# Kernel optimization log

Hardware: AMD Instinct MI355X
Metric: run time of the kernel (lower is better)

Reference implementation:

```python
import jax, jax.numpy as jnp
import numpy as np

N, E, F, H, G, C = 50000, 800000, 128, 64, 512, 10
RATIO = 0.5  # forward arg `ratio` baked as constant


def seg_mean(msgs, idx, n):
    s = jax.ops.segment_sum(msgs, idx, num_segments=n)
    cnt = jax.ops.segment_sum(jnp.ones(idx.shape[0], msgs.dtype), idx, num_segments=n)
    return s / jnp.maximum(cnt, 1.0)[:, None]


def sage(x, src, dst, Wl, bl, Wr, ew=None):
    # PyG SAGEConv: lin_l(mean_{j->i} msg_j) + lin_r(x_i); weighted variant scales messages
    m = x[src] if ew is None else x[src] * ew[:, None]
    agg = seg_mean(m, dst, x.shape[0])
    return agg @ Wl + bl + x @ Wr


def topk_mask(scores, seg, num_graphs, ratio):
    # per-graph (segment) top-k edge selection: keep ceil(ratio*edges_in_graph) highest scores
    e = scores.shape[0]
    counts = jax.ops.segment_sum(jnp.ones(e, jnp.float32), seg, num_segments=num_graphs)
    order = jnp.lexsort((-scores, seg))  # sort by segment, then score descending
    seg_sorted = seg[order]
    starts = jnp.concatenate([jnp.zeros(1, jnp.float32), jnp.cumsum(counts)[:-1]])
    rank = jnp.arange(e, dtype=jnp.float32) - starts[seg_sorted]
    k = jnp.ceil(ratio * counts)
    sel = (rank < k[seg_sorted]).astype(scores.dtype)
    return jnp.zeros(e, scores.dtype).at[order].set(sel)


def setup_inputs():
    key = jax.random.key(0)
    ks = jax.random.split(key, 16)
    w = lambda k, shape, fan: (jax.random.normal(k, shape, jnp.float32) / np.sqrt(fan))
    return {
        'x': jax.random.normal(ks[0], (N, F), jnp.float32),
        'edge_index': jax.random.randint(ks[1], (2, E), 0, N, jnp.int32),
        'batch': jnp.sort(jax.random.randint(ks[2], (N,), 0, G, jnp.int32)),
        'W1l': w(ks[3], (F, H), F), 'b1l': jnp.zeros(H, jnp.float32), 'W1r': w(ks[4], (F, H), F),
        'W2l': w(ks[5], (H, H), H), 'b2l': jnp.zeros(H, jnp.float32), 'W2r': w(ks[6], (H, H), H),
        'W3l': w(ks[7], (H, H), H), 'b3l': jnp.zeros(H, jnp.float32), 'W3r': w(ks[8], (H, H), H),
        'Wlin1': w(ks[9], (H, H), H), 'blin1': jnp.zeros(H, jnp.float32),
        'Wlin2': w(ks[10], (H, C), H), 'blin2': jnp.zeros(C, jnp.float32),
    }


def reference(x, edge_index, batch, W1l, b1l, W1r, W2l, b2l, W2r, W3l, b3l, W3r, Wlin1, blin1, Wlin2, blin2):
    src, dst = edge_index[0], edge_index[1]
    h = jax.nn.relu(sage(x, src, dst, W1l, b1l, W1r))
    edge_scores = jnp.sum(h[src] * h[dst], axis=-1)  # [E]
    seg = batch[src]  # graph id per edge (sections)
    sampled = topk_mask(edge_scores, seg, G, RATIO)
    ew = edge_scores * sampled
    h = jax.nn.relu(sage(h, src, dst, W2l, b2l, W2r, ew))
    h = jax.nn.relu(sage(h, src, dst, W3l, b3l, W3r, ew))
    pooled = seg_mean(h, batch, G)  # global_mean_pool
    z = jax.nn.relu(pooled @ Wlin1 + blin1)
    z = z @ Wlin2 + blin2  # dropout inactive in eval
    return jax.nn.log_softmax(z, axis=-1), sampled
```

## Files before the change

kernel.cpp:

```cpp
#include <hip/hip_runtime.h>
#include <hip/hip_bf16.h>
#include <math.h>

static constexpr int N = 50000;
static constexpr int E = 800000;
static constexpr int F = 128;
static constexpr int H = 64;
static constexpr int G = 512;
static constexpr int C = 10;
static constexpr int CAP = 256;

static inline int cdiv(long a, int b) { return (int)((a + b - 1) / b); }

__device__ __forceinline__ float uinv_score(unsigned u) {
  return (u & 0x80000000u) ? __uint_as_float(u & 0x7fffffffu) : __uint_as_float(~u);
}

__global__ void k_deg_goff(const int* __restrict__ dst, const int* __restrict__ batch,
                           int* __restrict__ deg, int* __restrict__ goff) {
  for (int i = blockIdx.x * 256 + threadIdx.x; i < N; i += gridDim.x * 256) {
    int b = batch[i];
    if (i == 0) {
      for (int g = 0; g <= b; ++g) goff[g] = 0;
    } else {
      int p = batch[i - 1];
      for (int g = p + 1; g <= b; ++g) goff[g] = i;
    }
    if (i == N - 1) {
      for (int g = b + 1; g <= G; ++g) goff[g] = N;
    }
  }
  for (int e = blockIdx.x * 256 + threadIdx.x; e < E; e += gridDim.x * 256)
    atomicAdd(&deg[dst[e]], 1);
}

__global__ void k_scan_a(const int* __restrict__ cnt, int* __restrict__ off,
                         int* __restrict__ bsum, int n) {
  __shared__ int wsum[16];
  int tid = threadIdx.x, lane = tid & 63, wv = tid >> 6;
  int idx = blockIdx.x * 4096 + tid * 4;
  int v0 = (idx + 0 < n) ? cnt[idx + 0] : 0;
  int v1 = (idx + 1 < n) ? cnt[idx + 1] : 0;
  int v2 = (idx + 2 < n) ? cnt[idx + 2] : 0;
  int v3 = (idx + 3 < n) ? cnt[idx + 3] : 0;
  int local = v0 + v1 + v2 + v3;
  int inc = local;
  for (int d = 1; d < 64; d <<= 1) {
    int t = __shfl_up(inc, d);
    if (lane >= d) inc += t;
  }
  if (lane == 63) wsum[wv] = inc;
  __syncthreads();
  if (tid < 16) {
    int t = wsum[tid];
    for (int d = 1; d < 16; d <<= 1) {
      int u = __shfl_up(t, d);
      if (tid >= d) t += u;
    }
    wsum[tid] = t;
  }
  __syncthreads();
  int woff = (wv > 0) ? wsum[wv - 1] : 0;
  int excl = woff + inc - local;
  if (idx + 0 < n) off[idx + 0] = excl;
  if (idx + 1 < n) off[idx + 1] = excl + v0;
  if (idx + 2 < n) off[idx + 2] = excl + v0 + v1;
  if (idx + 3 < n) off[idx + 3] = excl + v0 + v1 + v2;
  if (tid == 0) bsum[blockIdx.x] = wsum[15];
}

__global__ void k_scan_b(int* __restrict__ bsum, int nb) {
  int lane = threadIdx.x;
  int v = (lane < nb) ? bsum[lane] : 0;
  int inc = v;
  for (int d = 1; d < 64; d <<= 1) {
    int t = __shfl_up(inc, d);
    if (lane >= d) inc += t;
  }
  if (lane < nb) bsum[lane] = inc - v;
  if (lane == nb) bsum[nb] = inc;
}

__global__ void k_scan_c(int* __restrict__ off, int* __restrict__ cursor,
                         const int* __restrict__ bsum, int n, int nb) {
  int i = blockIdx.x * 256 + threadIdx.x;
  if (i < n) {
    int v = off[i] + bsum[i >> 12];
    off[i] = v;
    cursor[i] = v;
  } else if (i == n) {
    off[n] = bsum[nb];
  }
}

__global__ void k_fill_csr(const int* __restrict__ src, const int* __restrict__ dst,
                           int* __restrict__ cursor, int2* __restrict__ csr,
                           int* __restrict__ einv, int lo, int hi) {
  int e = blockIdx.x * 256 + threadIdx.x;
  if (e >= E) return;
  int d = dst[e];
  if (d < lo || d >= hi) return;
  int slot = atomicAdd(&cursor[d], 1);
  csr[slot] = make_int2(src[e], e);
  einv[e] = slot;
}

template <int K>
__global__ void k_gemm2(const float* __restrict__ in, const float* __restrict__ Wl,
                        const float* __restrict__ Wr, const float* __restrict__ b,
                        float* __restrict__ y, float* __restrict__ r) {
  __shared__ float sx[16][K];
  int lane = threadIdx.x, ty = threadIdx.y;
  int tid = ty * 64 + lane;
  int row0 = blockIdx.x * 16;
  const float4* gsrc = (const float4*)(in + (size_t)row0 * K);
  float4* sdst = (float4*)(&sx[0][0]);
#pragma unroll
  for (int i = tid; i < 16 * K / 4; i += 256) sdst[i] = gsrc[i];
  __syncthreads();
  float al[4], ar[4];
  float bias = b[lane];
#pragma unroll
  for (int j = 0; j < 4; ++j) { al[j] = 0.f; ar[j] = bias; }
#pragma unroll 4
  for (int f = 0; f < K; ++f) {
    float wl = Wl[f * H + lane];
    float wr = Wr[f * H + lane];
#pragma unroll
    for (int j = 0; j < 4; ++j) {
      float xv = sx[ty * 4 + j][f];
      al[j] += xv * wl;
      ar[j] += xv * wr;
    }
  }
#pragma unroll
  for (int j = 0; j < 4; ++j) {
    int row = row0 + ty * 4 + j;
    y[(size_t)row * H + lane] = al[j];
    r[(size_t)row * H + lane] = ar[j];
  }
}

template <int K>
__global__ void k_gemm2h(const float* __restrict__ in, const float* __restrict__ Wl,
                         const float* __restrict__ Wr, const float* __restrict__ b,
                         __hip_bfloat16* __restrict__ y, float* __restrict__ r) {
  __shared__ float sx[16][K];
  int lane = threadIdx.x, ty = threadIdx.y;
  int tid = ty * 64 + lane;
  int row0 = blockIdx.x * 16;
  const float4* gsrc = (const float4*)(in + (size_t)row0 * K);
  float4* sdst = (float4*)(&sx[0][0]);
#pragma unroll
  for (int i = tid; i < 16 * K / 4; i += 256) sdst[i] = gsrc[i];
  __syncthreads();
  float al[4], ar[4];
  float bias = b[lane];
#pragma unroll
  for (int j = 0; j < 4; ++j) { al[j] = 0.f; ar[j] = bias; }
#pragma unroll 4
  for (int f = 0; f < K; ++f) {
    float wl = Wl[f * H + lane];
    float wr = Wr[f * H + lane];
#pragma unroll
    for (int j = 0; j < 4; ++j) {
      float xv = sx[ty * 4 + j][f];
      al[j] += xv * wl;
      ar[j] += xv * wr;
    }
  }
#pragma unroll
  for (int j = 0; j < 4; ++j) {
    int row = row0 + ty * 4 + j;
    y[(size_t)row * H + lane] = __float2bfloat16(al[j]);
    r[(size_t)row * H + lane] = ar[j];
  }
}

__global__ void k_agg1(const float* __restrict__ y, const float* __restrict__ r,
                       const int2* __restrict__ csr, const int* __restrict__ off,
                       float* __restrict__ out) {
  int node = blockIdx.x * 8 + threadIdx.y;
  int lane = threadIdx.x;
  int q = lane >> 3, c = lane & 7;
  int s0 = off[node], s1 = off[node + 1];
  float4 a0 = make_float4(0.f, 0.f, 0.f, 0.f);
  float4 a1 = make_float4(0.f, 0.f, 0.f, 0.f);
  int i = s0 + q;
  for (; i + 8 < s1; i += 16) {
    int2 se0 = csr[i];
    int2 se1 = csr[i + 8];
    const float4* p0 = (const float4*)(y + (size_t)se0.x * H);
    const float4* p1 = (const float4*)(y + (size_t)se1.x * H);
    float4 u0 = p0[c], v0 = p0[c + 8];
    float4 u1 = p1[c], v1 = p1[c + 8];
    a0.x += u0.x + u1.x; a0.y += u0.y + u1.y; a0.z += u0.z + u1.z; a0.w += u0.w + u1.w;
    a1.x += v0.x + v1.x; a1.y += v0.y + v1.y; a1.z += v0.z + v1.z; a1.w += v0.w + v1.w;
  }
  for (; i < s1; i += 8) {
    int2 se = csr[i];
    const float4* p = (const float4*)(y + (size_t)se.x * H);
    float4 u = p[c], v = p[c + 8];
    a0.x += u.x; a0.y += u.y; a0.z += u.z; a0.w += u.w;
    a1.x += v.x; a1.y += v.y; a1.z += v.z; a1.w += v.w;
  }
#pragma unroll
  for (int d = 8; d < 64; d <<= 1) {
    a0.x += __shfl_xor(a0.x, d); a0.y += __shfl_xor(a0.y, d);
    a0.z += __shfl_xor(a0.z, d); a0.w += __shfl_xor(a0.w, d);
    a1.x += __shfl_xor(a1.x, d); a1.y += __shfl_xor(a1.y, d);
    a1.z += __shfl_xor(a1.z, d); a1.w += __shfl_xor(a1.w, d);
  }
  if (q == 0) {
    float inv = 1.f / fmaxf((float)(s1 - s0), 1.f);
    const float4* rp = (const float4*)(r + (size_t)node * H);
    float4 r0 = rp[c], r1 = rp[c + 8];
    float4 o0, o1;
    o0.x = fmaxf(a0.x * inv + r0.x, 0.f); o0.y = fmaxf(a0.y * inv + r0.y, 0.f);
    o0.z = fmaxf(a0.z * inv + r0.z, 0.f); o0.w = fmaxf(a0.w * inv + r0.w, 0.f);
    o1.x = fmaxf(a1.x * inv + r1.x, 0.f); o1.y = fmaxf(a1.y * inv + r1.y, 0.f);
    o1.z = fmaxf(a1.z * inv + r1.z, 0.f); o1.w = fmaxf(a1.w * inv + r1.w, 0.f);
    float4* op = (float4*)(out + (size_t)node * H);
    op[c] = o0; op[c + 8] = o1;
  }
}

__global__ void k_compact(const unsigned char* __restrict__ sel,
                          const int2* __restrict__ csr, const float* __restrict__ ewc,
                          const int* __restrict__ off, int2* __restrict__ csr2,
                          int* __restrict__ cnt2) {
  int node = blockIdx.x * 8 + threadIdx.y;
  int lane = threadIdx.x;
  int s0 = off[node], s1 = off[node + 1];
  unsigned long long lt = ((unsigned long long)1 << lane) - 1;
  int cum = 0;
  for (int i0 = s0; i0 < s1; i0 += 64) {
    int i = i0 + lane;
    bool f = (i < s1) && sel[i];
    unsigned long long m = __ballot(f);
    if (f) {
      int rank = __popcll(m & lt);
      int2 se = csr[i];
      csr2[s0 + cum + rank] = make_int2(se.x, __float_as_int(ewc[i]));
    }
    cum += __popcll(m);
  }
  if (lane == 0) cnt2[node] = cum;
}

__global__ void k_agg_w(const __hip_bfloat16* __restrict__ y, const float* __restrict__ r,
                        const int2* __restrict__ csr2, const int* __restrict__ cnt2,
                        const int* __restrict__ off, float* __restrict__ out) {
  int node = blockIdx.x * 8 + threadIdx.y;
  int lane = threadIdx.x;
  int q = lane >> 3, c = lane & 7;
  int b0 = off[node], cn = cnt2[node];
  float a[8] = {0.f, 0.f, 0.f, 0.f, 0.f, 0.f, 0.f, 0.f};
  for (int j = q; j < cn; j += 8) {
    int2 sw = csr2[b0 + j];
    float w = __int_as_float(sw.y);
    uint4 pk = ((const uint4*)((const unsigned short*)y + (size_t)sw.x * H))[c];
    a[0] += w * __uint_as_float(pk.x << 16); a[1] += w * __uint_as_float(pk.x & 0xffff0000u);
    a[2] += w * __uint_as_float(pk.y << 16); a[3] += w * __uint_as_float(pk.y & 0xffff0000u);
    a[4] += w * __uint_as_float(pk.z << 16); a[5] += w * __uint_as_float(pk.z & 0xffff0000u);
    a[6] += w * __uint_as_float(pk.w << 16); a[7] += w * __uint_as_float(pk.w & 0xffff0000u);
  }
#pragma unroll
  for (int d = 8; d < 64; d <<= 1) {
#pragma unroll
    for (int j = 0; j < 8; ++j) a[j] += __shfl_xor(a[j], d);
  }
  if (q == 0) {
    int degn = off[node + 1] - off[node];
    float inv = 1.f / fmaxf((float)degn, 1.f);
    const float4* rp = (const float4*)(r + (size_t)node * H);
    float4 r0 = rp[2 * c], r1 = rp[2 * c + 1];
    float4 o0, o1;
    o0.x = fmaxf(a[0] * inv + r0.x, 0.f); o0.y = fmaxf(a[1] * inv + r0.y, 0.f);
    o0.z = fmaxf(a[2] * inv + r0.z, 0.f); o0.w = fmaxf(a[3] * inv + r0.w, 0.f);
    o1.x = fmaxf(a[4] * inv + r1.x, 0.f); o1.y = fmaxf(a[5] * inv + r1.y, 0.f);
    o1.z = fmaxf(a[6] * inv + r1.z, 0.f); o1.w = fmaxf(a[7] * inv + r1.w, 0.f);
    float4* op = (float4*)(out + (size_t)node * H);
    op[2 * c] = o0; op[2 * c + 1] = o1;
  }
}

__global__ void k_score_csr(const float* __restrict__ h1, const int2* __restrict__ csr,
                            const int* __restrict__ off, const int* __restrict__ batch,
                            unsigned* __restrict__ scoreu_csr,
                            unsigned short* __restrict__ seg_csr, int* __restrict__ hist) {
  int node = blockIdx.x * 8 + threadIdx.y;
  int lane = threadIdx.x;
  int q = lane >> 4, c = lane & 15;
  int s0 = off[node], s1 = off[node + 1];
  float4 hn = ((const float4*)(h1 + (size_t)node * H))[c];
  int i = s0 + q;
  for (; i + 4 < s1; i += 8) {
    int2 se0 = csr[i];
    int2 se1 = csr[i + 4];
    float4 hs0 = ((const float4*)(h1 + (size_t)se0.x * H))[c];
    float4 hs1 = ((const float4*)(h1 + (size_t)se1.x * H))[c];
    float p0 = hn.x * hs0.x + hn.y * hs0.y + hn.z * hs0.z + hn.w * hs0.w;
    float p1 = hn.x * hs1.x + hn.y * hs1.y + hn.z * hs1.z + hn.w * hs1.w;
    p0 += __shfl_xor(p0, 1); p1 += __shfl_xor(p1, 1);
    p0 += __shfl_xor(p0, 2); p1 += __shfl_xor(p1, 2);
    p0 += __shfl_xor(p0, 4); p1 += __shfl_xor(p1, 4);
    p0 += __shfl_xor(p0, 8); p1 += __shfl_xor(p1, 8);
    if (c == 0) {
      int g0 = batch[se0.x], g1 = batch[se1.x];
      unsigned u0 = __float_as_uint(p0); u0 = (u0 & 0x80000000u) ? ~u0 : (u0 | 0x80000000u);
      unsigned u1 = __float_as_uint(p1); u1 = (u1 & 0x80000000u) ? ~u1 : (u1 | 0x80000000u);
      scoreu_csr[i] = u0; scoreu_csr[i + 4] = u1;
      seg_csr[i] = (unsigned short)g0; seg_csr[i + 4] = (unsigned short)g1;
      atomicAdd(&hist[g0 * 256 + (int)(u0 >> 24)], 1);
      atomicAdd(&hist[g1 * 256 + (int)(u1 >> 24)], 1);
    }
  }
  for (; i < s1; i += 4) {
    int2 se = csr[i];
    float4 hs = ((const float4*)(h1 + (size_t)se.x * H))[c];
    float p = hn.x * hs.x + hn.y * hs.y + hn.z * hs.z + hn.w * hs.w;
    p += __shfl_xor(p, 1);
    p += __shfl_xor(p, 2);
    p += __shfl_xor(p, 4);
    p += __shfl_xor(p, 8);
    if (c == 0) {
      int g = batch[se.x];
      unsigned u = __float_as_uint(p);
      u = (u & 0x80000000u) ? ~u : (u | 0x80000000u);
      scoreu_csr[i] = u;
      seg_csr[i] = (unsigned short)g;
      atomicAdd(&hist[g * 256 + (int)(u >> 24)], 1);
    }
  }
}

__global__ void k_hist(const unsigned* __restrict__ scoreu, const unsigned short* __restrict__ seg,
                       const unsigned* __restrict__ prefix, int* __restrict__ hist, int pass) {
  int e = blockIdx.x * 256 + threadIdx.x;
  if (e >= E) return;
  unsigned u = scoreu[e];
  int g = (int)seg[e];
  int predshift = 32 - 8 * pass;
  if ((u >> predshift) == (prefix[g] >> predshift))
    atomicAdd(&hist[g * 256 + (int)((u >> (24 - 8 * pass)) & 0xFFu)], 1);
}

__global__ void k_scan(int* __restrict__ hist, unsigned* __restrict__ prefix,
                       int* __restrict__ krem, int pass) {
  int g = blockIdx.x;
  int lane = threadIdx.x;
  int4* row = (int4*)(hist + (size_t)g * 256);
  int4 v = row[lane];
  int vj[4] = {v.x, v.y, v.z, v.w};
  int s = v.x + v.y + v.z + v.w;
  int inc = s;
  for (int d = 1; d < 64; d <<= 1) {
    int t = __shfl_up(inc, d);
    if (lane >= d) inc += t;
  }
  int T = __shfl(inc, 63);
  int k = (pass == 0) ? ((T + 1) >> 1) : krem[g];
  int excl = inc - s;
  int pre[4] = {excl, excl + vj[0], excl + vj[0] + vj[1], excl + vj[0] + vj[1] + vj[2]};
  int bsel_l = -1, newk_l = 0;
  if (k > 0) {
    for (int j = 3; j >= 0; --j) {
      int suf = T - pre[j];
      if (suf >= k) { bsel_l = 4 * lane + j; newk_l = k - (suf - vj[j]); break; }
    }
  }
  unsigned long long mask = __ballot(bsel_l >= 0);
  int bsel = 255, newk = 0;
  if (k > 0 && mask) {
    int hi = 63 - __builtin_clzll(mask);
    bsel = __shfl(bsel_l, hi);
    newk = __shfl(newk_l, hi);
  }
  if (lane == 0) {
    unsigned base = (pass == 0) ? 0u : prefix[g];
    prefix[g] = base | ((unsigned)bsel << (24 - 8 * pass));
    krem[g] = newk;
  }
  row[lane] = make_int4(0, 0, 0, 0);
}

__global__ void k_select(const unsigned* __restrict__ scoreu_csr,
                         const unsigned short* __restrict__ seg_csr,
                         const unsigned* __restrict__ thresh,
                         int* __restrict__ eqcnt, int* __restrict__ eqlist,
                         unsigned char* __restrict__ sel_csr, float* __restrict__ ew_csr) {
  int s = blockIdx.x * 256 + threadIdx.x;
  if (s >= E) return;
  unsigned u = scoreu_csr[s];
  int g = (int)seg_csr[s];
  unsigned t = thresh[g];
  unsigned um = u & 0xffffff00u;
  float sel = 0.f;
  if (um > t) sel = 1.f;
  else if (um == t) {
    int slot = atomicAdd(&eqcnt[g], 1);
    if (slot < CAP) eqlist[g * CAP + slot] = s;
  }
  sel_csr[s] = (unsigned char)sel;
  ew_csr[s] = uinv_score(u) * sel;
}

__global__ void k_resolve(const int* __restrict__ krem, const int* __restrict__ eqcnt,
                          const int* __restrict__ eqlist, const int2* __restrict__ csr,
                          const unsigned* __restrict__ scoreu_csr,
                          unsigned char* __restrict__ sel_csr, float* __restrict__ ew_csr) {
  int g = blockIdx.x * 256 + threadIdx.x;
  if (g >= G) return;
  int c = eqcnt[g]; if (c > CAP) c = CAP;
  int r = krem[g];  if (r > c) r = c;
  const int* lst = eqlist + g * CAP;
  unsigned last_u = 0u; int last_e = -1; bool first = true;
  for (int i = 0; i < r; ++i) {
    unsigned bu = 0u; int be = -1, bs = -1;
    for (int j = 0; j < c; ++j) {
      int slot = lst[j];
      unsigned u = scoreu_csr[slot];
      int eid = csr[slot].y;
      bool after = first || (u < last_u) || (u == last_u && eid > last_e);
      if (after && (bs < 0 || u > bu || (u == bu && eid < be))) { bu = u; be = eid; bs = slot; }
    }
    if (bs < 0) break;
    sel_csr[bs] = 1;
    ew_csr[bs] = uinv_score(bu);
    last_u = bu; last_e = be; first = false;
  }
}

__global__ void k_sampled(const int* __restrict__ einv, const unsigned char* __restrict__ sel_csr,
                          float* __restrict__ sampled) {
  int e = (blockIdx.x * 256 + threadIdx.x) * 4;
  if (e >= E) return;
  int4 iv = *(const int4*)(einv + e);
  float4 o;
  o.x = (float)sel_csr[iv.x];
  o.y = (float)sel_csr[iv.y];
  o.z = (float)sel_csr[iv.z];
  o.w = (float)sel_csr[iv.w];
  *(float4*)(sampled + e) = o;
}

__global__ void k_poolhead(const float* __restrict__ h3, const int* __restrict__ goff,
                           const float* __restrict__ W1, const float* __restrict__ b1,
                           const float* __restrict__ W2, const float* __restrict__ b2,
                           float* __restrict__ outp) {
  int g = blockIdx.x;
  int h = threadIdx.x;
  int s0 = goff[g], s1 = goff[g + 1];
  float a = 0.f;
  for (int n = s0; n < s1; ++n) a += h3[(size_t)n * H + h];
  float inv = 1.f / fmaxf((float)(s1 - s0), 1.f);
  __shared__ float p[H], z1[H], z2[C];
  __shared__ float lse;
  p[h] = a * inv;
  __syncthreads();
  float acc = b1[h];
#pragma unroll 8
  for (int f = 0; f < H; ++f) acc += p[f] * W1[f * H + h];
  z1[h] = fmaxf(acc, 0.f);
  __syncthreads();
  if (h < C) {
    float a2 = b2[h];
#pragma unroll 8
    for (int f = 0; f < H; ++f) a2 += z1[f] * W2[f * C + h];
    z2[h] = a2;
  }
  __syncthreads();
  if (h == 0) {
    float m = z2[0];
    for (int c = 1; c < C; ++c) m = fmaxf(m, z2[c]);
    float s = 0.f;
    for (int c = 0; c < C; ++c) s += expf(z2[c] - m);
    lse = m + logf(s);
  }
  __syncthreads();
  if (h < C) outp[(size_t)g * C + h] = z2[h] - lse;
}

extern "C" void kernel_launch(void* const* d_in, const int* in_sizes, int n_in,
                              void* d_out, int out_size, void* d_ws, size_t ws_size,
                              hipStream_t stream) {
  const float* x     = (const float*)d_in[0];
  const int*   ei    = (const int*)d_in[1];
  const int*   batch = (const int*)d_in[2];
  const float* W1l   = (const float*)d_in[3];
  const float* b1l   = (const float*)d_in[4];
  const float* W1r   = (const float*)d_in[5];
  const float* W2l   = (const float*)d_in[6];
  const float* b2l   = (const float*)d_in[7];
  const float* W2r   = (const float*)d_in[8];
  const float* W3l   = (const float*)d_in[9];
  const float* b3l   = (const float*)d_in[10];
  const float* W3r   = (const float*)d_in[11];
  const float* Wlin1 = (const float*)d_in[12];
  const float* blin1 = (const float*)d_in[13];
  const float* Wlin2 = (const float*)d_in[14];
  const float* blin2 = (const float*)d_in[15];

  const int* srcv = ei;
  const int* dstv = ei + E;

  float* out_ls   = (float*)d_out;
  float* out_samp = out_ls + G * C;

  char* w = (char*)d_ws;
  auto carve = [&](size_t bytes) { void* p = (void*)w; w += (bytes + 255) & ~(size_t)255; return p; };
  char* zbase   = w;
  int*      deg     = (int*)carve((size_t)N * 4);
  int*      eqcnt   = (int*)carve((size_t)G * 4);
  int*      hist    = (int*)carve((size_t)G * 256 * 4);
  size_t    zbytes  = (size_t)(w - zbase);
  float*    h1      = (float*)carve((size_t)N * H * 4);
  float*    h2      = (float*)carve((size_t)N * H * 4);
  float*    h3      = (float*)carve((size_t)N * H * 4);
  float*    yb      = (float*)carve((size_t)N * H * 4);
  float*    rb      = (float*)carve((size_t)N * H * 4);
  __hip_bfloat16* ybh = (__hip_bfloat16*)carve((size_t)N * H * 2);
  unsigned* scoreu_csr = (unsigned*)carve((size_t)E * 4);
  unsigned short* seg_csr = (unsigned short*)carve((size_t)E * 2);
  float*    ew_csr     = (float*)carve((size_t)E * 4);
  unsigned char* sel_csr = (unsigned char*)carve((size_t)E);
  int2*     csr     = (int2*)carve((size_t)E * 8);
  int*      einv    = (int*)carve((size_t)E * 4);
  int*      off     = (int*)carve((size_t)(N + 1) * 4);
  int*      cursor  = (int*)carve((size_t)N * 4);
  int*      cnt2    = (int*)carve((size_t)N * 4);
  int*      goff    = (int*)carve((size_t)(G + 1) * 4);
  unsigned* prefix  = (unsigned*)carve((size_t)G * 4);
  int*      krem    = (int*)carve((size_t)G * 4);
  int*      eqlist  = (int*)carve((size_t)G * CAP * 4);
  int*      bsum    = (int*)carve((size_t)16 * 4);
  int2*     csr2    = (int2*)carve((size_t)E * 8);

  hipMemsetAsync(zbase, 0, zbytes, stream);

  k_deg_goff<<<128, 256, 0, stream>>>(dstv, batch, deg, goff);
  int nb = cdiv(N, 4096);
  k_scan_a<<<nb, 1024, 0, stream>>>(deg, off, bsum, N);
  k_scan_b<<<1, 64, 0, stream>>>(bsum, nb);
  k_scan_c<<<cdiv(N + 1, 256), 256, 0, stream>>>(off, cursor, bsum, N, nb);
  k_fill_csr<<<cdiv(E, 256), 256, 0, stream>>>(srcv, dstv, cursor, csr, einv, 0, N / 2);
  k_fill_csr<<<cdiv(E, 256), 256, 0, stream>>>(srcv, dstv, cursor, csr, einv, N / 2, N);

  k_gemm2<F><<<N / 16, dim3(64, 4), 0, stream>>>(x, W1l, W1r, b1l, yb, rb);
  k_agg1<<<N / 8, dim3(64, 8), 0, stream>>>(yb, rb, csr, off, h1);

  k_score_csr<<<N / 8, dim3(64, 8), 0, stream>>>(h1, csr, off, batch,
                                                 scoreu_csr, seg_csr, hist);
  k_scan<<<G, 64, 0, stream>>>(hist, prefix, krem, 0);
  for (int p = 1; p <= 2; ++p) {
    k_hist<<<cdiv(E, 256), 256, 0, stream>>>(scoreu_csr, seg_csr, prefix, hist, p);
    k_scan<<<G, 64, 0, stream>>>(hist, prefix, krem, p);
  }
  k_select<<<cdiv(E, 256), 256, 0, stream>>>(scoreu_csr, seg_csr, prefix,
                                             eqcnt, eqlist, sel_csr, ew_csr);
  k_resolve<<<cdiv(G, 256), 256, 0, stream>>>(krem, eqcnt, eqlist, csr, scoreu_csr,
                                              sel_csr, ew_csr);
  k_sampled<<<cdiv(E / 4, 256), 256, 0, stream>>>(einv, sel_csr, out_samp);

  k_compact<<<N / 8, dim3(64, 8), 0, stream>>>(sel_csr, csr, ew_csr, off, csr2, cnt2);

  k_gemm2h<H><<<N / 16, dim3(64, 4), 0, stream>>>(h1, W2l, W2r, b2l, ybh, rb);
  k_agg_w<<<N / 8, dim3(64, 8), 0, stream>>>(ybh, rb, csr2, cnt2, off, h2);

  k_gemm2h<H><<<N / 16, dim3(64, 4), 0, stream>>>(h2, W3l, W3r, b3l, ybh, rb);
  k_agg_w<<<N / 8, dim3(64, 8), 0, stream>>>(ybh, rb, csr2, cnt2, off, h3);

  k_poolhead<<<G, 64, 0, stream>>>(h3, goff, Wlin1, blin1, Wlin2, blin2, out_ls);
}
```

Measured before the change: 499.2 us.

## Parallelize edge scoring over edges and scatter sampled mask in select

Edge scoring now runs one 16-lane group per four edges over the flat CSR array instead of one warp per destination node. Each edge looks up its destination through a new dsts array filled during CSR construction, which removes load imbalance from skewed node degrees. The separate k_sampled kernel and the einv array are dropped: k_select and k_resolve scatter the sampled value directly to the original edge index. The cost is an extra gather of the destination row per edge, since the node row is no longer reused across a node's edges, plus scattered 4-byte writes.

```diff
diff --git a/kernel.cpp b/kernel.cpp
--- a/kernel.cpp
+++ b/kernel.cpp
@@ -95,14 +95,14 @@
 
 __global__ void k_fill_csr(const int* __restrict__ src, const int* __restrict__ dst,
                            int* __restrict__ cursor, int2* __restrict__ csr,
-                           int* __restrict__ einv, int lo, int hi) {
+                           int* __restrict__ dsts, int lo, int hi) {
   int e = blockIdx.x * 256 + threadIdx.x;
   if (e >= E) return;
   int d = dst[e];
   if (d < lo || d >= hi) return;
   int slot = atomicAdd(&cursor[d], 1);
   csr[slot] = make_int2(src[e], e);
-  einv[e] = slot;
+  dsts[slot] = d;
 }
 
 template <int K>
@@ -286,52 +286,47 @@
 }
 
 __global__ void k_score_csr(const float* __restrict__ h1, const int2* __restrict__ csr,
-                            const int* __restrict__ off, const int* __restrict__ batch,
+                            const int* __restrict__ dsts, const int* __restrict__ batch,
                             unsigned* __restrict__ scoreu_csr,
                             unsigned short* __restrict__ seg_csr, int* __restrict__ hist) {
-  int node = blockIdx.x * 8 + threadIdx.y;
   int lane = threadIdx.x;
   int q = lane >> 4, c = lane & 15;
-  int s0 = off[node], s1 = off[node + 1];
-  float4 hn = ((const float4*)(h1 + (size_t)node * H))[c];
-  int i = s0 + q;
-  for (; i + 4 < s1; i += 8) {
-    int2 se0 = csr[i];
-    int2 se1 = csr[i + 4];
-    float4 hs0 = ((const float4*)(h1 + (size_t)se0.x * H))[c];
-    float4 hs1 = ((const float4*)(h1 + (size_t)se1.x * H))[c];
-    float p0 = hn.x * hs0.x + hn.y * hs0.y + hn.z * hs0.z + hn.w * hs0.w;
-    float p1 = hn.x * hs1.x + hn.y * hs1.y + hn.z * hs1.z + hn.w * hs1.w;
-    p0 += __shfl_xor(p0, 1); p1 += __shfl_xor(p1, 1);
-    p0 += __shfl_xor(p0, 2); p1 += __shfl_xor(p1, 2);
-    p0 += __shfl_xor(p0, 4); p1 += __shfl_xor(p1, 4);
-    p0 += __shfl_xor(p0, 8); p1 += __shfl_xor(p1, 8);
-    if (c == 0) {
-      int g0 = batch[se0.x], g1 = batch[se1.x];
-      unsigned u0 = __float_as_uint(p0); u0 = (u0 & 0x80000000u) ? ~u0 : (u0 | 0x80000000u);
-      unsigned u1 = __float_as_uint(p1); u1 = (u1 & 0x80000000u) ? ~u1 : (u1 | 0x80000000u);
-      scoreu_csr[i] = u0; scoreu_csr[i + 4] = u1;
-      seg_csr[i] = (unsigned short)g0; seg_csr[i + 4] = (unsigned short)g1;
-      atomicAdd(&hist[g0 * 256 + (int)(u0 >> 24)], 1);
-      atomicAdd(&hist[g1 * 256 + (int)(u1 >> 24)], 1);
-    }
-  }
-  for (; i < s1; i += 4) {
-    int2 se = csr[i];
-    float4 hs = ((const float4*)(h1 + (size_t)se.x * H))[c];
-    float p = hn.x * hs.x + hn.y * hs.y + hn.z * hs.z + hn.w * hs.w;
-    p += __shfl_xor(p, 1);
-    p += __shfl_xor(p, 2);
-    p += __shfl_xor(p, 4);
-    p += __shfl_xor(p, 8);
-    if (c == 0) {
-      int g = batch[se.x];
-      unsigned u = __float_as_uint(p);
-      u = (u & 0x80000000u) ? ~u : (u | 0x80000000u);
-      scoreu_csr[i] = u;
-      seg_csr[i] = (unsigned short)g;
-      atomicAdd(&hist[g * 256 + (int)(u >> 24)], 1);
-    }
+  int s = (blockIdx.x * 8 + threadIdx.y) * 16 + q * 4;
+  int2 e0 = csr[s + 0], e1 = csr[s + 1], e2 = csr[s + 2], e3 = csr[s + 3];
+  int d0 = dsts[s + 0], d1 = dsts[s + 1], d2 = dsts[s + 2], d3 = dsts[s + 3];
+  float4 x0 = ((const float4*)(h1 + (size_t)e0.x * H))[c];
+  float4 x1 = ((const float4*)(h1 + (size_t)e1.x * H))[c];
+  float4 x2 = ((const float4*)(h1 + (size_t)e2.x * H))[c];
+  float4 x3 = ((const float4*)(h1 + (size_t)e3.x * H))[c];
+  float4 y0 = ((const float4*)(h1 + (size_t)d0 * H))[c];
+  float4 y1 = ((const float4*)(h1 + (size_t)d1 * H))[c];
+  float4 y2 = ((const float4*)(h1 + (size_t)d2 * H))[c];
+  float4 y3 = ((const float4*)(h1 + (size_t)d3 * H))[c];
+  float p0 = y0.x * x0.x + y0.y * x0.y + y0.z * x0.z + y0.w * x0.w;
+  float p1 = y1.x * x1.x + y1.y * x1.y + y1.z * x1.z + y1.w * x1.w;
+  float p2 = y2.x * x2.x + y2.y * x2.y + y2.z * x2.z + y2.w * x2.w;
+  float p3 = y3.x * x3.x + y3.y * x3.y + y3.z * x3.z + y3.w * x3.w;
+#pragma unroll
+  for (int d = 1; d < 16; d <<= 1) {
+    p0 += __shfl_xor(p0, d);
+    p1 += __shfl_xor(p1, d);
+    p2 += __shfl_xor(p2, d);
+    p3 += __shfl_xor(p3, d);
+  }
+  if (c == 0) {
+    int g0 = batch[e0.x], g1 = batch[e1.x], g2 = batch[e2.x], g3 = batch[e3.x];
+    unsigned u0 = __float_as_uint(p0); u0 = (u0 & 0x80000000u) ? ~u0 : (u0 | 0x80000000u);
+    unsigned u1 = __float_as_uint(p1); u1 = (u1 & 0x80000000u) ? ~u1 : (u1 | 0x80000000u);
+    unsigned u2 = __float_as_uint(p2); u2 = (u2 & 0x80000000u) ? ~u2 : (u2 | 0x80000000u);
+    unsigned u3 = __float_as_uint(p3); u3 = (u3 & 0x80000000u) ? ~u3 : (u3 | 0x80000000u);
+    scoreu_csr[s + 0] = u0; scoreu_csr[s + 1] = u1;
+    scoreu_csr[s + 2] = u2; scoreu_csr[s + 3] = u3;
+    seg_csr[s + 0] = (unsigned short)g0; seg_csr[s + 1] = (unsigned short)g1;
+    seg_csr[s + 2] = (unsigned short)g2; seg_csr[s + 3] = (unsigned short)g3;
+    atomicAdd(&hist[g0 * 256 + (int)(u0 >> 24)], 1);
+    atomicAdd(&hist[g1 * 256 + (int)(u1 >> 24)], 1);
+    atomicAdd(&hist[g2 * 256 + (int)(u2 >> 24)], 1);
+    atomicAdd(&hist[g3 * 256 + (int)(u3 >> 24)], 1);
   }
 }
 
@@ -387,9 +382,10 @@
 
 __global__ void k_select(const unsigned* __restrict__ scoreu_csr,
                          const unsigned short* __restrict__ seg_csr,
-                         const unsigned* __restrict__ thresh,
+                         const unsigned* __restrict__ thresh, const int2* __restrict__ csr,
                          int* __restrict__ eqcnt, int* __restrict__ eqlist,
-                         unsigned char* __restrict__ sel_csr, float* __restrict__ ew_csr) {
+                         unsigned char* __restrict__ sel_csr, float* __restrict__ ew_csr,
+                         float* __restrict__ sampled) {
   int s = blockIdx.x * 256 + threadIdx.x;
   if (s >= E) return;
   unsigned u = scoreu_csr[s];
@@ -404,12 +400,14 @@
   }
   sel_csr[s] = (unsigned char)sel;
   ew_csr[s] = uinv_score(u) * sel;
+  sampled[csr[s].y] = sel;
 }
 
 __global__ void k_resolve(const int* __restrict__ krem, const int* __restrict__ eqcnt,
                           const int* __restrict__ eqlist, const int2* __restrict__ csr,
                           const unsigned* __restrict__ scoreu_csr,
-                          unsigned char* __restrict__ sel_csr, float* __restrict__ ew_csr) {
+                          unsigned char* __restrict__ sel_csr, float* __restrict__ ew_csr,
+                          float* __restrict__ sampled) {
   int g = blockIdx.x * 256 + threadIdx.x;
   if (g >= G) return;
   int c = eqcnt[g]; if (c > CAP) c = CAP;
@@ -428,21 +426,9 @@
     if (bs < 0) break;
     sel_csr[bs] = 1;
     ew_csr[bs] = uinv_score(bu);
+    sampled[be] = 1.f;
     last_u = bu; last_e = be; first = false;
   }
-}
-
-__global__ void k_sampled(const int* __restrict__ einv, const unsigned char* __restrict__ sel_csr,
-                          float* __restrict__ sampled) {
-  int e = (blockIdx.x * 256 + threadIdx.x) * 4;
-  if (e >= E) return;
-  int4 iv = *(const int4*)(einv + e);
-  float4 o;
-  o.x = (float)sel_csr[iv.x];
-  o.y = (float)sel_csr[iv.y];
-  o.z = (float)sel_csr[iv.z];
-  o.w = (float)sel_csr[iv.w];
-  *(float4*)(sampled + e) = o;
 }
 
 __global__ void k_poolhead(const float* __restrict__ h3, const int* __restrict__ goff,
@@ -526,7 +512,7 @@
   float*    ew_csr     = (float*)carve((size_t)E * 4);
   unsigned char* sel_csr = (unsigned char*)carve((size_t)E);
   int2*     csr     = (int2*)carve((size_t)E * 8);
-  int*      einv    = (int*)carve((size_t)E * 4);
+  int*      dsts    = (int*)carve((size_t)E * 4);
   int*      off     = (int*)carve((size_t)(N + 1) * 4);
   int*      cursor  = (int*)carve((size_t)N * 4);
   int*      cnt2    = (int*)carve((size_t)N * 4);
@@ -544,24 +530,23 @@
   k_scan_a<<<nb, 1024, 0, stream>>>(deg, off, bsum, N);
   k_scan_b<<<1, 64, 0, stream>>>(bsum, nb);
   k_scan_c<<<cdiv(N + 1, 256), 256, 0, stream>>>(off, cursor, bsum, N, nb);
-  k_fill_csr<<<cdiv(E, 256), 256, 0, stream>>>(srcv, dstv, cursor, csr, einv, 0, N / 2);
-  k_fill_csr<<<cdiv(E, 256), 256, 0, stream>>>(srcv, dstv, cursor, csr, einv, N / 2, N);
+  k_fill_csr<<<cdiv(E, 256), 256, 0, stream>>>(srcv, dstv, cursor, csr, dsts, 0, N / 2);
+  k_fill_csr<<<cdiv(E, 256), 256, 0, stream>>>(srcv, dstv, cursor, csr, dsts, N / 2, N);
 
   k_gemm2<F><<<N / 16, dim3(64, 4), 0, stream>>>(x, W1l, W1r, b1l, yb, rb);
   k_agg1<<<N / 8, dim3(64, 8), 0, stream>>>(yb, rb, csr, off, h1);
 
-  k_score_csr<<<N / 8, dim3(64, 8), 0, stream>>>(h1, csr, off, batch,
-                                                 scoreu_csr, seg_csr, hist);
+  k_score_csr<<<E / 128, dim3(64, 8), 0, stream>>>(h1, csr, dsts, batch,
+                                                   scoreu_csr, seg_csr, hist);
   k_scan<<<G, 64, 0, stream>>>(hist, prefix, krem, 0);
   for (int p = 1; p <= 2; ++p) {
     k_hist<<<cdiv(E, 256), 256, 0, stream>>>(scoreu_csr, seg_csr, prefix, hist, p);
     k_scan<<<G, 64, 0, stream>>>(hist, prefix, krem, p);
   }
-  k_select<<<cdiv(E, 256), 256, 0, stream>>>(scoreu_csr, seg_csr, prefix,
-                                             eqcnt, eqlist, sel_csr, ew_csr);
+  k_select<<<cdiv(E, 256), 256, 0, stream>>>(scoreu_csr, seg_csr, prefix, csr,
+                                             eqcnt, eqlist, sel_csr, ew_csr, out_samp);
   k_resolve<<<cdiv(G, 256), 256, 0, stream>>>(krem, eqcnt, eqlist, csr, scoreu_csr,
-                                              sel_csr, ew_csr);
-  k_sampled<<<cdiv(E / 4, 256), 256, 0, stream>>>(einv, sel_csr, out_samp);
+                                              sel_csr, ew_csr, out_samp);
 
   k_compact<<<N / 8, dim3(64, 8), 0, stream>>>(sel_csr, csr, ew_csr, off, csr2, cnt2);
 
```

Measured after the change: 498.6 us. About the same (-0.1%).
